# Kernel optimization log

Hardware: AMD Instinct MI355X
Metric: run time of the kernel (lower is better)

## Reference

```python
import jax, jax.numpy as jnp
import numpy as np

B, N, S, D, H = 64, 4096, 8, 256, 512
ITERS = 3
EPS = 1e-8      # slot-attention renormalize epsilon
LN_EPS = 1e-5   # torch LayerNorm default


def _ln(x, g, b):
    m = jnp.mean(x, -1, keepdims=True)
    v = jnp.mean((x - m) ** 2, -1, keepdims=True)
    return (x - m) * jax.lax.rsqrt(v + LN_EPS) * g + b


def setup_inputs() -> dict:
    key = jax.random.key(0)
    ks = jax.random.split(key, 12)

    def xav(k, shape):
        s = (6.0 / (shape[-2] + shape[-1])) ** 0.5
        return jax.random.uniform(k, shape, jnp.float32, -s, s)

    gru_s = 1.0 / (D ** 0.5)
    return {
        "inputs": jax.random.normal(ks[0], (B, N, D), jnp.float32),
        "init_noise": jax.random.normal(ks[1], (B, S, D), jnp.float32),
        "slots_mu": xav(ks[2], (1, 1, D)),
        "slots_log_sigma": xav(ks[3], (1, 1, D)),
        "ln_in_g": jnp.ones(D), "ln_in_b": jnp.zeros(D),
        "ln_slots_g": jnp.ones(D), "ln_slots_b": jnp.zeros(D),
        "ln_mlp_g": jnp.ones(D), "ln_mlp_b": jnp.zeros(D),
        "Wq": xav(ks[4], (D, D)),
        "Wk": xav(ks[5], (D, D)),
        "Wv": xav(ks[6], (D, D)),
        "W_ih": jax.random.uniform(ks[7], (3 * D, D), jnp.float32, -gru_s, gru_s),
        "W_hh": jax.random.uniform(ks[8], (3 * D, D), jnp.float32, -gru_s, gru_s),
        "b_ih": jnp.zeros(3 * D), "b_hh": jnp.zeros(3 * D),
        "W1": xav(ks[9], (H, D)), "b1": jnp.zeros(H),
        "W2": xav(ks[10], (D, H)), "b2": jnp.zeros(D),
    }


def reference(inputs, init_noise, slots_mu, slots_log_sigma,
              ln_in_g, ln_in_b, ln_slots_g, ln_slots_b, ln_mlp_g, ln_mlp_b,
              Wq, Wk, Wv, W_ih, W_hh, b_ih, b_hh, W1, b1, W2, b2):
    x = _ln(inputs, ln_in_g, ln_in_b)               # (B,N,D)
    k = jnp.einsum('bnd,ed->bne', x, Wk)             # (B,N,D)
    v = jnp.einsum('bnd,ed->bne', x, Wv)             # (B,N,D)
    slots = slots_mu + jnp.exp(slots_log_sigma) * init_noise  # (B,S,D)
    scale = D ** (-0.5)
    for _ in range(ITERS):
        prev = slots
        s = _ln(slots, ln_slots_g, ln_slots_b)
        q = jnp.einsum('bsd,ed->bse', s, Wq) * scale
        logits = jnp.einsum('bse,bne->bsn', q, k)    # (B,S,N)
        attn = jax.nn.softmax(logits, -1) + EPS
        attn = attn / jnp.sum(attn, -1, keepdims=True)
        upd = jnp.einsum('bsn,bne->bse', attn, v)    # (B,S,D)
        # GRUCell (torch semantics)
        gx = jnp.einsum('bsd,ed->bse', upd, W_ih) + b_ih
        gh = jnp.einsum('bsd,ed->bse', prev, W_hh) + b_hh
        xr, xz, xn = jnp.split(gx, 3, -1)
        hr, hz, hn = jnp.split(gh, 3, -1)
        r = jax.nn.sigmoid(xr + hr)
        z = jax.nn.sigmoid(xz + hz)
        n = jnp.tanh(xn + r * hn)
        slots = (1.0 - z) * n + z * prev
        # residual MLP
        m = _ln(slots, ln_mlp_g, ln_mlp_b)
        h1 = jax.nn.relu(jnp.einsum('bsd,hd->bsh', m, W1) + b1)
        slots = slots + jnp.einsum('bsh,dh->bsd', h1, W2) + b2
    return slots
```

## Files before the change

### kernel.cpp

```cpp
#include <hip/hip_runtime.h>

#define BB 64
#define NN 4096
#define SS 8
#define DD 256
#define HH 512
#define NCH 16
#define CHK 256
#define LSP2 260

typedef __attribute__((ext_vector_type(4))) float f32x4;
typedef __attribute__((ext_vector_type(8))) short short8;
typedef __attribute__((ext_vector_type(8))) __bf16 bf16x8;

static __device__ __forceinline__ f32x4 MFMA(short8 a, short8 b, f32x4 c){
  return __builtin_amdgcn_mfma_f32_16x16x32_bf16(
      __builtin_bit_cast(bf16x8, a), __builtin_bit_cast(bf16x8, b), c, 0, 0, 0);
}

static __device__ __forceinline__ unsigned short f2bf(float f){
  unsigned int x = __builtin_bit_cast(unsigned int, f);
  x += 0x7FFFu + ((x >> 16) & 1u);
  return (unsigned short)(x >> 16);
}

static __device__ __forceinline__ unsigned int pk2(float a, float b){
  return (unsigned int)f2bf(a) | ((unsigned int)f2bf(b) << 16);
}

__global__ __launch_bounds__(256, 4) void pre_kernel(
    const float* __restrict__ Wq, const float* __restrict__ Wk,
    const float* __restrict__ Wih, const float* __restrict__ Wv,
    float* __restrict__ wqkT, float* __restrict__ mf32)
{
  __shared__ float sh[256];
  const int blk = blockIdx.x, t = threadIdx.x;
  if(blk < 256){
    const int d2 = blk;
    sh[t] = Wk[(size_t)t * 256 + d2];
    __syncthreads();
    float acc = 0.f;
    #pragma unroll 8
    for(int e = 0; e < 256; ++e) acc += sh[e] * Wq[(size_t)e * 256 + t];
    wqkT[(size_t)d2 * 256 + t] = acc * 0.0625f;
  } else {
    const int e = blk - 256;
    sh[t] = Wih[(size_t)e * 256 + t];
    __syncthreads();
    float acc = 0.f;
    #pragma unroll 8
    for(int d = 0; d < 256; ++d) acc += sh[d] * Wv[(size_t)d * 256 + t];
    mf32[(size_t)e * 256 + t] = acc;
  }
}

struct PackDesc {
  const float* src[5];
  unsigned short* dst[5];
  int ET[5];
  int K[5];
  int blkStart[6];
};

__global__ void pack_all_kernel(PackDesc pd){
  int blk = blockIdx.x;
  int seg = 0;
  #pragma unroll
  for(int i = 1; i < 5; ++i) if(blk >= pd.blkStart[i]) seg = i;
  int tid = (blk - pd.blkStart[seg]) * 256 + threadIdx.x;
  int ET = pd.ET[seg], K = pd.K[seg];
  if(tid >= ET * 16 * K) return;
  int i    = tid & 7;
  int lane = (tid >> 3) & 63;
  int rest = tid >> 9;
  int et = rest % ET;
  int kk = rest / ET;
  int row = et * 16 + (lane & 15);
  int col = kk * 32 + ((lane >> 4) << 3) + i;
  pd.dst[seg][tid] = f2bf(pd.src[seg][(size_t)row * K + col]);
}

__global__ __launch_bounds__(256, 4) void ln_kernel(
    const float* __restrict__ inp, const float* __restrict__ g, const float* __restrict__ bta,
    unsigned short* __restrict__ x)
{
  const int t = threadIdx.x, w = t >> 6, l = t & 63;
  const size_t row0 = (size_t)blockIdx.x * 64;
  const int li = l & 15, lg = l >> 4;

  float4 gg[4], bb[4];
  #pragma unroll
  for(int q = 0; q < 4; ++q){
    gg[q] = ((const float4*)g)[li + q * 16];
    bb[q] = ((const float4*)bta)[li + q * 16];
  }
  #pragma unroll
  for(int rr = 0; rr < 4; ++rr){
    int r = w * 16 + rr * 4 + lg;
    const float4* rp = (const float4*)(inp + (row0 + r) * DD);
    float4 xv[4];
    #pragma unroll
    for(int q = 0; q < 4; ++q) xv[q] = rp[li + q * 16];
    float s1 = 0.f, s2 = 0.f;
    #pragma unroll
    for(int q = 0; q < 4; ++q){
      s1 += xv[q].x + xv[q].y + xv[q].z + xv[q].w;
      s2 += xv[q].x*xv[q].x + xv[q].y*xv[q].y + xv[q].z*xv[q].z + xv[q].w*xv[q].w;
    }
    #pragma unroll
    for(int o = 8; o >= 1; o >>= 1){ s1 += __shfl_xor(s1, o); s2 += __shfl_xor(s2, o); }
    float mean = s1 * (1.0f/256.0f);
    float inv  = rsqrtf(s2 * (1.0f/256.0f) - mean*mean + 1e-5f);
    #pragma unroll
    for(int q = 0; q < 4; ++q){
      float y0 = (xv[q].x-mean)*inv*gg[q].x + bb[q].x;
      float y1 = (xv[q].y-mean)*inv*gg[q].y + bb[q].y;
      float y2 = (xv[q].z-mean)*inv*gg[q].z + bb[q].z;
      float y3 = (xv[q].w-mean)*inv*gg[q].w + bb[q].w;
      *(uint2*)((char*)x + (row0 + r) * 512 + q * 128 + li * 8) =
          make_uint2(pk2(y0,y1), pk2(y2,y3));
    }
  }
}

__global__ __launch_bounds__(256, 1) void init_kernel(
    const float* __restrict__ noise, const float* __restrict__ mu, const float* __restrict__ lsg,
    const float* __restrict__ lng, const float* __restrict__ lnb,
    const short8* __restrict__ wqkp, float* __restrict__ slots, float* __restrict__ qbuf)
{
  const int b = blockIdx.x, t = threadIdx.x, w = t >> 6, l = t & 63;
  __shared__ float SLN[SS * DD];
  __shared__ unsigned short A1[16 * DD];
  float muv = mu[t];
  float sgv = __expf(lsg[t]);
  #pragma unroll
  for(int s = 0; s < SS; ++s){
    float v = muv + sgv * noise[(size_t)b * 2048 + s * 256 + t];
    slots[(size_t)b * 2048 + s * 256 + t] = v;
    SLN[s * 256 + t] = v;
  }
  __syncthreads();
  float4 g4 = ((const float4*)lng)[l], bb4 = ((const float4*)lnb)[l];
  for(int sh = 0; sh < 2; ++sh){
    int s = w * 2 + sh;
    float4 x4 = ((const float4*)(SLN + s * 256))[l];
    float s1 = x4.x + x4.y + x4.z + x4.w;
    float s2 = x4.x*x4.x + x4.y*x4.y + x4.z*x4.z + x4.w*x4.w;
    #pragma unroll
    for(int o = 32; o >= 1; o >>= 1){ s1 += __shfl_xor(s1, o); s2 += __shfl_xor(s2, o); }
    float mean = s1 * (1.0f/256.0f);
    float inv  = rsqrtf(s2 * (1.0f/256.0f) - mean*mean + 1e-5f);
    float y0 = (x4.x-mean)*inv*g4.x + bb4.x;
    float y1 = (x4.y-mean)*inv*g4.y + bb4.y;
    float y2 = (x4.z-mean)*inv*g4.z + bb4.z;
    float y3 = (x4.w-mean)*inv*g4.w + bb4.w;
    int byte = s * 512 + ((l * 8) ^ ((s & 7) << 4));
    *(uint2*)((char*)A1 + byte) = make_uint2(pk2(y0,y1), pk2(y2,y3));
  }
  __syncthreads();
  const int m = l & 15;
  short8 af[8];
  #pragma unroll
  for(int kk = 0; kk < 8; ++kk){
    int ab = m * 512 + (((kk * 64) + ((l >> 4) << 4)) ^ ((m & 7) << 4));
    af[kk] = *(const short8*)((const char*)A1 + ab);
  }
  #pragma unroll
  for(int i = 0; i < 4; ++i){
    int et = w + i * 4;
    f32x4 c = (f32x4){0,0,0,0};
    #pragma unroll
    for(int kk = 0; kk < 8; ++kk) c = MFMA(af[kk], wqkp[((kk * 16 + et) << 6) + l], c);
    int e = et * 16 + (l & 15);
    #pragma unroll
    for(int j = 0; j < 4; ++j){
      int s = ((l >> 4) << 2) + j;
      if(s < 8) qbuf[(size_t)b * 2048 + s * 256 + e] = c[j];
    }
  }
}

__global__ __launch_bounds__(256, 3) void attn_kernel(
    const unsigned short* __restrict__ x_, const float* __restrict__ qbuf,
    float* __restrict__ pupd, float* __restrict__ pms)
{
  const int blk = blockIdx.x;
  const int b = blk >> 4, c = blk & 15;
  const int t = threadIdx.x, w = t >> 6, l = t & 63;
  __shared__ __align__(16) char SMEM[32768];
  float* ls = (float*)SMEM;
  char*  xv = SMEM;

  const int m = l & 15, lg = l >> 4;
  short8 aq[8];
  #pragma unroll
  for(int kk = 0; kk < 8; ++kk){
    if(m < 8){
      const float* qp = qbuf + (size_t)b * 2048 + m * 256 + kk * 32 + (lg << 3);
      float4 qa = *(const float4*)qp;
      float4 qb = *(const float4*)(qp + 4);
      int4 pv = make_int4((int)pk2(qa.x,qa.y), (int)pk2(qa.z,qa.w),
                          (int)pk2(qb.x,qb.y), (int)pk2(qb.z,qb.w));
      aq[kk] = __builtin_bit_cast(short8, pv);
    } else {
      aq[kk] = (short8){0,0,0,0,0,0,0,0};
    }
  }

  const unsigned short* xb = x_ + ((size_t)b * NN + (size_t)c * CHK) * DD;
  #pragma unroll
  for(int nt = 0; nt < 4; ++nt){
    int nb = w * 64 + nt * 16;
    f32x4 acc = (f32x4){0,0,0,0};
    #pragma unroll
    for(int kk = 0; kk < 8; ++kk){
      short8 bk = *(const short8*)(xb + (size_t)(nb + m) * DD + kk * 32 + (lg << 3));
      acc = MFMA(aq[kk], bk, acc);
    }
    if(l < 32){
      int s4 = lg * 4;
      #pragma unroll
      for(int j = 0; j < 4; ++j) ls[(s4 + j) * LSP2 + nb + m] = acc[j];
    }
  }
  __syncthreads();

  for(int sh = 0; sh < 2; ++sh){
    int s = w * 2 + sh;
    float* base = ls + s * LSP2;
    float4 v0 = *(float4*)(base + l * 4);
    float mx = fmaxf(fmaxf(v0.x,v0.y),fmaxf(v0.z,v0.w));
    #pragma unroll
    for(int o = 32; o >= 1; o >>= 1) mx = fmaxf(mx, __shfl_xor(mx, o));
    float e0 = __expf(v0.x-mx), e1 = __expf(v0.y-mx), e2 = __expf(v0.z-mx), e3 = __expf(v0.w-mx);
    float sm = e0+e1+e2+e3;
    #pragma unroll
    for(int o = 32; o >= 1; o >>= 1) sm += __shfl_xor(sm, o);
    *(float4*)(base + l * 4) = make_float4(e0,e1,e2,e3);
    if(l == 0){
      pms[(((size_t)b * 16 + c) * 8 + s) * 2    ] = mx;
      pms[(((size_t)b * 16 + c) * 8 + s) * 2 + 1] = sm;
    }
  }
  __syncthreads();

  short8 pa[8];
  #pragma unroll
  for(int kk = 0; kk < 8; ++kk){
    if(m < 8){
      const float* pp = ls + m * LSP2 + kk * 32 + (lg << 3);
      int4 pv = make_int4((int)pk2(pp[0],pp[1]), (int)pk2(pp[2],pp[3]),
                          (int)pk2(pp[4],pp[5]), (int)pk2(pp[6],pp[7]));
      pa[kk] = __builtin_bit_cast(short8, pv);
    } else {
      pa[kk] = (short8){0,0,0,0,0,0,0,0};
    }
  }
  __syncthreads();

  f32x4 acc[4];
  #pragma unroll
  for(int dt = 0; dt < 4; ++dt) acc[dt] = (f32x4){0,0,0,0};
  const int p = t & 31, db = t >> 5;

  uint4 va0, va1, va2, va3, vb0, vb1, vb2, vb3;
  {
    const unsigned short* rA = xb + (size_t)(2 * p) * DD + db * 32;
    const unsigned short* rB = rA + DD;
    va0 = *(const uint4*)(rA);      vb0 = *(const uint4*)(rB);
    va1 = *(const uint4*)(rA + 8);  vb1 = *(const uint4*)(rB + 8);
    va2 = *(const uint4*)(rA + 16); vb2 = *(const uint4*)(rB + 16);
    va3 = *(const uint4*)(rA + 24); vb3 = *(const uint4*)(rB + 24);
  }

  for(int ng = 0; ng < 4; ++ng){
    {
      uint4 VA[4] = {va0, va1, va2, va3};
      uint4 VB[4] = {vb0, vb1, vb2, vb3};
      #pragma unroll
      for(int q = 0; q < 4; ++q){
        unsigned int wa[4] = {VA[q].x, VA[q].y, VA[q].z, VA[q].w};
        unsigned int wb[4] = {VB[q].x, VB[q].y, VB[q].z, VB[q].w};
        #pragma unroll
        for(int h = 0; h < 4; ++h){
          int d0 = db * 32 + q * 8 + h * 2;
          unsigned int a = wa[h], bv = wb[h];
          unsigned int v0 = (a & 0xFFFFu) | (bv << 16);
          unsigned int v1 = (a >> 16) | (bv & 0xFFFF0000u);
          *(unsigned int*)(xv + d0 * 128 + ((p * 4) ^ ((d0 & 7) << 4))) = v0;
          int d1 = d0 + 1;
          *(unsigned int*)(xv + d1 * 128 + ((p * 4) ^ ((d1 & 7) << 4))) = v1;
        }
      }
    }
    if(ng < 3){
      const unsigned short* rA = xb + (size_t)((ng + 1) * 64 + 2 * p) * DD + db * 32;
      const unsigned short* rB = rA + DD;
      va0 = *(const uint4*)(rA);      vb0 = *(const uint4*)(rB);
      va1 = *(const uint4*)(rA + 8);  vb1 = *(const uint4*)(rB + 8);
      va2 = *(const uint4*)(rA + 16); vb2 = *(const uint4*)(rB + 16);
      va3 = *(const uint4*)(rA + 24); vb3 = *(const uint4*)(rB + 24);
    }
    __builtin_amdgcn_s_setprio(1);
    #pragma unroll
    for(int kkloc = 0; kkloc < 2; ++kkloc){
      int kk = ng * 2 + kkloc;
      #pragma unroll
      for(int dt = 0; dt < 4; ++dt){
        int d = w * 64 + dt * 16 + m;
        short8 bv = *(const short8*)(xv + d * 128 + ((kkloc * 64 + lg * 16) ^ ((d & 7) << 4)));
        acc[dt] = MFMA(pa[kk], bv, acc[dt]);
      }
    }
    __builtin_amdgcn_s_setprio(0);
  }
  if(l < 32){
    int s4 = lg * 4;
    #pragma unroll
    for(int dt = 0; dt < 4; ++dt){
      int d0 = w * 64 + dt * 16;
      #pragma unroll
      for(int j = 0; j < 4; ++j)
        pupd[((size_t)b * 16 + c) * 2048 + (s4 + j) * 256 + d0 + m] = acc[dt][j];
    }
  }
}

__global__ __launch_bounds__(1024, 1) void update_kernel(
    const float* __restrict__ pupd, const float* __restrict__ pms,
    float* __restrict__ slots, float* __restrict__ qbuf,
    const short8* __restrict__ mp, const short8* __restrict__ whh,
    const float* __restrict__ bih, const float* __restrict__ bhh,
    const short8* __restrict__ w1p, const float* __restrict__ b1v,
    const short8* __restrict__ w2p, const float* __restrict__ b2v,
    const float* __restrict__ lnsg, const float* __restrict__ lnsb,
    const float* __restrict__ lnmg, const float* __restrict__ lnmb,
    const short8* __restrict__ wqkp,
    float* __restrict__ dout, const int last)
{
  const int b = blockIdx.x, t = threadIdx.x, w = t >> 6, l = t & 63;
  __shared__ unsigned short A1[16 * 256];
  __shared__ unsigned short A2[16 * 256];
  __shared__ unsigned short A3[16 * 512];
  __shared__ float GR[8 * 256], GZ[8 * 256], GXN[8 * 256], GHN[8 * 256];
  __shared__ float SL[8 * 256];
  __shared__ float PMS[256];

  if(t < 256) PMS[t] = pms[(size_t)b * 256 + t];
  __syncthreads();

  const int col = t & 255, sg = t >> 8;
  float upd[2], pv[2];
  #pragma unroll
  for(int ss = 0; ss < 2; ++ss){
    int s = sg * 2 + ss;
    float mx = -1e30f;
    #pragma unroll
    for(int cc = 0; cc < 16; ++cc) mx = fmaxf(mx, PMS[(cc * 8 + s) * 2]);
    float Z = 0.f, u = 0.f;
    #pragma unroll
    for(int cc = 0; cc < 16; ++cc){
      float e = __expf(PMS[(cc * 8 + s) * 2] - mx);
      Z += e * PMS[(cc * 8 + s) * 2 + 1];
      u += e * pupd[((size_t)b * 16 + cc) * 2048 + s * 256 + col];
    }
    upd[ss] = u / Z;
    pv[ss]  = slots[(size_t)b * 2048 + s * 256 + col];
  }
  #pragma unroll
  for(int ss = 0; ss < 2; ++ss){
    int s = sg * 2 + ss;
    int byte = s * 512 + ((col * 2) ^ ((s & 7) << 4));
    *(unsigned short*)((char*)A1 + byte) = f2bf(upd[ss]);
    *(unsigned short*)((char*)A2 + byte) = f2bf(pv[ss]);
  }
  __syncthreads();

  {
    const int mq = l & 15;
    short8 a1f[8], a2f[8];
    #pragma unroll
    for(int kk = 0; kk < 8; ++kk){
      int ab = mq * 512 + (((kk * 64) + ((l >> 4) << 4)) ^ ((mq & 7) << 4));
      a1f[kk] = *(const short8*)((const char*)A1 + ab);
      a2f[kk] = *(const short8*)((const char*)A2 + ab);
    }
    #pragma unroll
    for(int i = 0; i < 3; ++i){
      int et = w + i * 16;
      f32x4 c1 = (f32x4){0,0,0,0}, c2 = (f32x4){0,0,0,0};
      #pragma unroll
      for(int kk = 0; kk < 8; ++kk){
        c1 = MFMA(a1f[kk], mp[((kk * 48 + et) << 6) + l], c1);
        c2 = MFMA(a2f[kk], whh[((kk * 48 + et) << 6) + l], c2);
      }
      int e = et * 16 + (l & 15);
      float xb = bih[e], hb = bhh[e];
      #pragma unroll
      for(int j = 0; j < 4; ++j){
        int s = ((l >> 4) << 2) + j;
        if(s < 8){
          float xx = c1[j] + xb, h = c2[j] + hb;
          if(i == 0)      GR[s * 256 + e      ] = 1.f/(1.f + __expf(-(xx + h)));
          else if(i == 1) GZ[s * 256 + (e-256)] = 1.f/(1.f + __expf(-(xx + h)));
          else { GXN[s * 256 + (e-512)] = xx; GHN[s * 256 + (e-512)] = h; }
        }
      }
    }
  }
  __syncthreads();

  #pragma unroll
  for(int ss = 0; ss < 2; ++ss){
    int s = sg * 2 + ss, idx = s * 256 + col;
    float r = GR[idx], z = GZ[idx], xn = GXN[idx], hn = GHN[idx];
    float nn = tanhf(xn + r * hn);
    SL[idx] = (1.f - z) * nn + z * pv[ss];
  }
  __syncthreads();

  if(w < 8){
    float4 g4 = ((const float4*)lnmg)[l], bb4 = ((const float4*)lnmb)[l];
    int s = w;
    float4 x4 = ((const float4*)(SL + s * 256))[l];
    float s1 = x4.x + x4.y + x4.z + x4.w;
    float s2 = x4.x*x4.x + x4.y*x4.y + x4.z*x4.z + x4.w*x4.w;
    #pragma unroll
    for(int o = 32; o >= 1; o >>= 1){ s1 += __shfl_xor(s1, o); s2 += __shfl_xor(s2, o); }
    float mean = s1 * (1.0f/256.0f);
    float inv  = rsqrtf(s2 * (1.0f/256.0f) - mean*mean + 1e-5f);
    float y0 = (x4.x-mean)*inv*g4.x + bb4.x;
    float y1 = (x4.y-mean)*inv*g4.y + bb4.y;
    float y2 = (x4.z-mean)*inv*g4.z + bb4.z;
    float y3 = (x4.w-mean)*inv*g4.w + bb4.w;
    int byte = s * 512 + ((l * 8) ^ ((s & 7) << 4));
    *(uint2*)((char*)A1 + byte) = make_uint2(pk2(y0,y1), pk2(y2,y3));
  }
  __syncthreads();

  {
    const int mq = l & 15;
    short8 af[8];
    #pragma unroll
    for(int kk = 0; kk < 8; ++kk){
      int ab = mq * 512 + (((kk * 64) + ((l >> 4) << 4)) ^ ((mq & 7) << 4));
      af[kk] = *(const short8*)((const char*)A1 + ab);
    }
    #pragma unroll
    for(int i = 0; i < 2; ++i){
      int et = w + i * 16;
      f32x4 cc = (f32x4){0,0,0,0};
      #pragma unroll
      for(int kk = 0; kk < 8; ++kk) cc = MFMA(af[kk], w1p[((kk * 32 + et) << 6) + l], cc);
      int e = et * 16 + (l & 15);
      float bb = b1v[e];
      #pragma unroll
      for(int j = 0; j < 4; ++j){
        int s = ((l >> 4) << 2) + j;
        if(s < 8){
          float h = fmaxf(cc[j] + bb, 0.f);
          int byte = s * 1024 + ((e * 2) ^ ((s & 7) << 4));
          *(unsigned short*)((char*)A3 + byte) = f2bf(h);
        }
      }
    }
  }
  __syncthreads();

  {
    const int mq = l & 15;
    short8 af[16];
    #pragma unroll
    for(int kk = 0; kk < 16; ++kk){
      int ab = mq * 1024 + (((kk * 64) + ((l >> 4) << 4)) ^ ((mq & 7) << 4));
      af[kk] = *(const short8*)((const char*)A3 + ab);
    }
    {
      int et = w;
      f32x4 cc = (f32x4){0,0,0,0};
      #pragma unroll
      for(int kk = 0; kk < 16; ++kk) cc = MFMA(af[kk], w2p[((kk * 16 + et) << 6) + l], cc);
      int e = et * 16 + (l & 15);
      float bb = b2v[e];
      #pragma unroll
      for(int j = 0; j < 4; ++j){
        int s = ((l >> 4) << 2) + j;
        if(s < 8) GR[s * 256 + e] = SL[s * 256 + e] + cc[j] + bb;
      }
    }
  }
  __syncthreads();

  for(int i = t; i < 2048; i += 1024){
    float v = GR[i];
    slots[(size_t)b * 2048 + i] = v;
    if(last) dout[(size_t)b * 2048 + i] = v;
  }
  if(w < 8){
    float4 g4 = ((const float4*)lnsg)[l], bb4 = ((const float4*)lnsb)[l];
    int s = w;
    float4 x4 = ((const float4*)(GR + s * 256))[l];
    float s1 = x4.x + x4.y + x4.z + x4.w;
    float s2 = x4.x*x4.x + x4.y*x4.y + x4.z*x4.z + x4.w*x4.w;
    #pragma unroll
    for(int o = 32; o >= 1; o >>= 1){ s1 += __shfl_xor(s1, o); s2 += __shfl_xor(s2, o); }
    float mean = s1 * (1.0f/256.0f);
    float inv  = rsqrtf(s2 * (1.0f/256.0f) - mean*mean + 1e-5f);
    float y0 = (x4.x-mean)*inv*g4.x + bb4.x;
    float y1 = (x4.y-mean)*inv*g4.y + bb4.y;
    float y2 = (x4.z-mean)*inv*g4.z + bb4.z;
    float y3 = (x4.w-mean)*inv*g4.w + bb4.w;
    int byte = s * 512 + ((l * 8) ^ ((s & 7) << 4));
    *(uint2*)((char*)A1 + byte) = make_uint2(pk2(y0,y1), pk2(y2,y3));
  }
  __syncthreads();
  {
    const int mq = l & 15;
    short8 af[8];
    #pragma unroll
    for(int kk = 0; kk < 8; ++kk){
      int ab = mq * 512 + (((kk * 64) + ((l >> 4) << 4)) ^ ((mq & 7) << 4));
      af[kk] = *(const short8*)((const char*)A1 + ab);
    }
    {
      int et = w;
      f32x4 cc = (f32x4){0,0,0,0};
      #pragma unroll
      for(int kk = 0; kk < 8; ++kk) cc = MFMA(af[kk], wqkp[((kk * 16 + et) << 6) + l], cc);
      int e = et * 16 + (l & 15);
      #pragma unroll
      for(int j = 0; j < 4; ++j){
        int s = ((l >> 4) << 2) + j;
        if(s < 8) qbuf[(size_t)b * 2048 + s * 256 + e] = cc[j];
      }
    }
  }
}

extern "C" void kernel_launch(void* const* d_in, const int* in_sizes, int n_in,
                              void* d_out, int out_size, void* d_ws, size_t ws_size,
                              hipStream_t stream)
{
  const float* inp   = (const float*)d_in[0];
  const float* noise = (const float*)d_in[1];
  const float* mu    = (const float*)d_in[2];
  const float* lsg   = (const float*)d_in[3];
  const float* lngi  = (const float*)d_in[4];
  const float* lnbi  = (const float*)d_in[5];
  const float* lngs  = (const float*)d_in[6];
  const float* lnbs  = (const float*)d_in[7];
  const float* lngm  = (const float*)d_in[8];
  const float* lnbm  = (const float*)d_in[9];
  const float* Wq    = (const float*)d_in[10];
  const float* Wk    = (const float*)d_in[11];
  const float* Wv    = (const float*)d_in[12];
  const float* Wih   = (const float*)d_in[13];
  const float* Whh   = (const float*)d_in[14];
  const float* bih   = (const float*)d_in[15];
  const float* bhh   = (const float*)d_in[16];
  const float* W1    = (const float*)d_in[17];
  const float* b1    = (const float*)d_in[18];
  const float* W2    = (const float*)d_in[19];
  const float* b2    = (const float*)d_in[20];
  float* dout = (float*)d_out;

  char* ws = (char*)d_ws;
  size_t off = 0;
  unsigned short* x   = (unsigned short*)(ws + off); off += (size_t)BB*NN*DD*2;
  short8* wqkp= (short8*)(ws + off); off += (size_t)256*256*2;
  short8* mp  = (short8*)(ws + off); off += (size_t)768*256*2;
  short8* whhp= (short8*)(ws + off); off += (size_t)768*256*2;
  short8* w1p = (short8*)(ws + off); off += (size_t)512*256*2;
  short8* w2p = (short8*)(ws + off); off += (size_t)256*512*2;
  float* wqkT = (float*)(ws + off);  off += (size_t)256*256*4;
  float* mf32 = (float*)(ws + off);  off += (size_t)768*256*4;
  float* qbuf = (float*)(ws + off);  off += (size_t)512*256*4;
  float* slots= (float*)(ws + off);  off += (size_t)512*256*4;
  float* pupd = (float*)(ws + off);  off += (size_t)BB*NCH*2048*4;
  float* pms  = (float*)(ws + off);  off += (size_t)BB*NCH*8*2*4;

  pre_kernel<<<1024, 256, 0, stream>>>(Wq, Wk, Wih, Wv, wqkT, mf32);

  PackDesc pd;
  const float* srcs[5] = {wqkT, mf32, Whh, W1, W2};
  unsigned short* dsts[5] = {(unsigned short*)wqkp, (unsigned short*)mp,
                             (unsigned short*)whhp, (unsigned short*)w1p,
                             (unsigned short*)w2p};
  int ets[5] = {16, 48, 48, 32, 16};
  int ks [5] = {256, 256, 256, 256, 512};
  int cum = 0;
  for(int i = 0; i < 5; ++i){
    pd.src[i] = srcs[i]; pd.dst[i] = dsts[i]; pd.ET[i] = ets[i]; pd.K[i] = ks[i];
    pd.blkStart[i] = cum;
    cum += (ets[i] * 16 * ks[i] + 255) / 256;
  }
  pd.blkStart[5] = cum;
  pack_all_kernel<<<cum, 256, 0, stream>>>(pd);

  ln_kernel<<<4096, 256, 0, stream>>>(inp, lngi, lnbi, x);
  init_kernel<<<64, 256, 0, stream>>>(noise, mu, lsg, lngs, lnbs, wqkp, slots, qbuf);

  for(int it = 0; it < 3; ++it){
    attn_kernel<<<BB * NCH, 256, 0, stream>>>(x, qbuf, pupd, pms);
    update_kernel<<<64, 1024, 0, stream>>>(pupd, pms, slots, qbuf, mp, whhp,
        bih, bhh, w1p, b1, w2p, b2, lngs, lnbs, lngm, lnbm, wqkp, dout, (it == 2) ? 1 : 0);
  }
}
```

Measured before the change: 338.2 us.

## Split attention over 64 chunks of 64 tokens per batch

Changes the split-softmax attention from 16 chunks of 256 tokens to 64 chunks of 64 tokens, so the attention grid grows from 1024 to 4096 blocks. Each block now does a single 16-row logits tile and a single staged V load, with no software-pipelined prefetch loop. The update kernel merges 64 partial max/sum/update sets instead of 16. This trades more launch parallelism and shorter per-block latency for four times the partial-update traffic written to and read back from global memory, plus a longer reduction in the update kernel.

```diff
diff --git a/kernel.cpp b/kernel.cpp
--- a/kernel.cpp
+++ b/kernel.cpp
@@ -5,9 +5,9 @@
 #define SS 8
 #define DD 256
 #define HH 512
-#define NCH 16
-#define CHK 256
-#define LSP2 260
+#define NCH 64
+#define CHK 64
+#define LSP3 68
 
 typedef __attribute__((ext_vector_type(4))) float f32x4;
 typedef __attribute__((ext_vector_type(8))) short short8;
@@ -185,7 +185,7 @@
     float* __restrict__ pupd, float* __restrict__ pms)
 {
   const int blk = blockIdx.x;
-  const int b = blk >> 4, c = blk & 15;
+  const int b = blk >> 6, c = blk & 63;
   const int t = threadIdx.x, w = t >> 6, l = t & 63;
   __shared__ __align__(16) char SMEM[32768];
   float* ls = (float*)SMEM;
@@ -208,9 +208,8 @@
   }
 
   const unsigned short* xb = x_ + ((size_t)b * NN + (size_t)c * CHK) * DD;
-  #pragma unroll
-  for(int nt = 0; nt < 4; ++nt){
-    int nb = w * 64 + nt * 16;
+  {
+    int nb = w * 16;
     f32x4 acc = (f32x4){0,0,0,0};
     #pragma unroll
     for(int kk = 0; kk < 8; ++kk){
@@ -220,35 +219,34 @@
     if(l < 32){
       int s4 = lg * 4;
       #pragma unroll
-      for(int j = 0; j < 4; ++j) ls[(s4 + j) * LSP2 + nb + m] = acc[j];
+      for(int j = 0; j < 4; ++j) ls[(s4 + j) * LSP3 + nb + m] = acc[j];
     }
   }
   __syncthreads();
 
   for(int sh = 0; sh < 2; ++sh){
     int s = w * 2 + sh;
-    float* base = ls + s * LSP2;
-    float4 v0 = *(float4*)(base + l * 4);
-    float mx = fmaxf(fmaxf(v0.x,v0.y),fmaxf(v0.z,v0.w));
+    float v = ls[s * LSP3 + l];
+    float mx = v;
     #pragma unroll
     for(int o = 32; o >= 1; o >>= 1) mx = fmaxf(mx, __shfl_xor(mx, o));
-    float e0 = __expf(v0.x-mx), e1 = __expf(v0.y-mx), e2 = __expf(v0.z-mx), e3 = __expf(v0.w-mx);
-    float sm = e0+e1+e2+e3;
+    float e0 = __expf(v - mx);
+    float sm = e0;
     #pragma unroll
     for(int o = 32; o >= 1; o >>= 1) sm += __shfl_xor(sm, o);
-    *(float4*)(base + l * 4) = make_float4(e0,e1,e2,e3);
+    ls[s * LSP3 + l] = e0;
     if(l == 0){
-      pms[(((size_t)b * 16 + c) * 8 + s) * 2    ] = mx;
-      pms[(((size_t)b * 16 + c) * 8 + s) * 2 + 1] = sm;
-    }
-  }
-  __syncthreads();
-
-  short8 pa[8];
-  #pragma unroll
-  for(int kk = 0; kk < 8; ++kk){
+      pms[(((size_t)b * 64 + c) * 8 + s) * 2    ] = mx;
+      pms[(((size_t)b * 64 + c) * 8 + s) * 2 + 1] = sm;
+    }
+  }
+  __syncthreads();
+
+  short8 pa[2];
+  #pragma unroll
+  for(int kk = 0; kk < 2; ++kk){
     if(m < 8){
-      const float* pp = ls + m * LSP2 + kk * 32 + (lg << 3);
+      const float* pp = ls + m * LSP3 + kk * 32 + (lg << 3);
       int4 pv = make_int4((int)pk2(pp[0],pp[1]), (int)pk2(pp[2],pp[3]),
                           (int)pk2(pp[4],pp[5]), (int)pk2(pp[6],pp[7]));
       pa[kk] = __builtin_bit_cast(short8, pv);
@@ -262,58 +260,42 @@
   #pragma unroll
   for(int dt = 0; dt < 4; ++dt) acc[dt] = (f32x4){0,0,0,0};
   const int p = t & 31, db = t >> 5;
-
-  uint4 va0, va1, va2, va3, vb0, vb1, vb2, vb3;
   {
     const unsigned short* rA = xb + (size_t)(2 * p) * DD + db * 32;
     const unsigned short* rB = rA + DD;
-    va0 = *(const uint4*)(rA);      vb0 = *(const uint4*)(rB);
-    va1 = *(const uint4*)(rA + 8);  vb1 = *(const uint4*)(rB + 8);
-    va2 = *(const uint4*)(rA + 16); vb2 = *(const uint4*)(rB + 16);
-    va3 = *(const uint4*)(rA + 24); vb3 = *(const uint4*)(rB + 24);
-  }
-
-  for(int ng = 0; ng < 4; ++ng){
-    {
-      uint4 VA[4] = {va0, va1, va2, va3};
-      uint4 VB[4] = {vb0, vb1, vb2, vb3};
-      #pragma unroll
-      for(int q = 0; q < 4; ++q){
-        unsigned int wa[4] = {VA[q].x, VA[q].y, VA[q].z, VA[q].w};
-        unsigned int wb[4] = {VB[q].x, VB[q].y, VB[q].z, VB[q].w};
-        #pragma unroll
-        for(int h = 0; h < 4; ++h){
-          int d0 = db * 32 + q * 8 + h * 2;
-          unsigned int a = wa[h], bv = wb[h];
-          unsigned int v0 = (a & 0xFFFFu) | (bv << 16);
-          unsigned int v1 = (a >> 16) | (bv & 0xFFFF0000u);
-          *(unsigned int*)(xv + d0 * 128 + ((p * 4) ^ ((d0 & 7) << 4))) = v0;
-          int d1 = d0 + 1;
-          *(unsigned int*)(xv + d1 * 128 + ((p * 4) ^ ((d1 & 7) << 4))) = v1;
-        }
+    uint4 VA[4], VB[4];
+    VA[0] = *(const uint4*)(rA);      VB[0] = *(const uint4*)(rB);
+    VA[1] = *(const uint4*)(rA + 8);  VB[1] = *(const uint4*)(rB + 8);
+    VA[2] = *(const uint4*)(rA + 16); VB[2] = *(const uint4*)(rB + 16);
+    VA[3] = *(const uint4*)(rA + 24); VB[3] = *(const uint4*)(rB + 24);
+    #pragma unroll
+    for(int q = 0; q < 4; ++q){
+      unsigned int wa[4] = {VA[q].x, VA[q].y, VA[q].z, VA[q].w};
+      unsigned int wb[4] = {VB[q].x, VB[q].y, VB[q].z, VB[q].w};
+      #pragma unroll
+      for(int h = 0; h < 4; ++h){
+        int d0 = db * 32 + q * 8 + h * 2;
+        unsigned int a = wa[h], bv = wb[h];
+        unsigned int v0 = (a & 0xFFFFu) | (bv << 16);
+        unsigned int v1 = (a >> 16) | (bv & 0xFFFF0000u);
+        *(unsigned int*)(xv + d0 * 128 + ((p * 4) ^ ((d0 & 7) << 4))) = v0;
+        int d1 = d0 + 1;
+        *(unsigned int*)(xv + d1 * 128 + ((p * 4) ^ ((d1 & 7) << 4))) = v1;
       }
     }
-    if(ng < 3){
-      const unsigned short* rA = xb + (size_t)((ng + 1) * 64 + 2 * p) * DD + db * 32;
-      const unsigned short* rB = rA + DD;
-      va0 = *(const uint4*)(rA);      vb0 = *(const uint4*)(rB);
-      va1 = *(const uint4*)(rA + 8);  vb1 = *(const uint4*)(rB + 8);
-      va2 = *(const uint4*)(rA + 16); vb2 = *(const uint4*)(rB + 16);
-      va3 = *(const uint4*)(rA + 24); vb3 = *(const uint4*)(rB + 24);
-    }
-    __builtin_amdgcn_s_setprio(1);
-    #pragma unroll
-    for(int kkloc = 0; kkloc < 2; ++kkloc){
-      int kk = ng * 2 + kkloc;
-      #pragma unroll
-      for(int dt = 0; dt < 4; ++dt){
-        int d = w * 64 + dt * 16 + m;
-        short8 bv = *(const short8*)(xv + d * 128 + ((kkloc * 64 + lg * 16) ^ ((d & 7) << 4)));
-        acc[dt] = MFMA(pa[kk], bv, acc[dt]);
-      }
-    }
-    __builtin_amdgcn_s_setprio(0);
-  }
+  }
+  __builtin_amdgcn_s_setprio(1);
+  #pragma unroll
+  for(int kkloc = 0; kkloc < 2; ++kkloc){
+    #pragma unroll
+    for(int dt = 0; dt < 4; ++dt){
+      int d = w * 64 + dt * 16 + m;
+      short8 bv = *(const short8*)(xv + d * 128 + ((kkloc * 64 + lg * 16) ^ ((d & 7) << 4)));
+      acc[dt] = MFMA(pa[kkloc], bv, acc[dt]);
+    }
+  }
+  __builtin_amdgcn_s_setprio(0);
+
   if(l < 32){
     int s4 = lg * 4;
     #pragma unroll
@@ -321,7 +303,7 @@
       int d0 = w * 64 + dt * 16;
       #pragma unroll
       for(int j = 0; j < 4; ++j)
-        pupd[((size_t)b * 16 + c) * 2048 + (s4 + j) * 256 + d0 + m] = acc[dt][j];
+        pupd[((size_t)b * 64 + c) * 2048 + (s4 + j) * 256 + d0 + m] = acc[dt][j];
     }
   }
 }
@@ -344,9 +326,9 @@
   __shared__ unsigned short A3[16 * 512];
   __shared__ float GR[8 * 256], GZ[8 * 256], GXN[8 * 256], GHN[8 * 256];
   __shared__ float SL[8 * 256];
-  __shared__ float PMS[256];
-
-  if(t < 256) PMS[t] = pms[(size_t)b * 256 + t];
+  __shared__ float PMS[1024];
+
+  PMS[t] = pms[(size_t)b * 1024 + t];
   __syncthreads();
 
   const int col = t & 255, sg = t >> 8;
@@ -355,14 +337,14 @@
   for(int ss = 0; ss < 2; ++ss){
     int s = sg * 2 + ss;
     float mx = -1e30f;
-    #pragma unroll
-    for(int cc = 0; cc < 16; ++cc) mx = fmaxf(mx, PMS[(cc * 8 + s) * 2]);
+    #pragma unroll 8
+    for(int cc = 0; cc < 64; ++cc) mx = fmaxf(mx, PMS[(cc * 8 + s) * 2]);
     float Z = 0.f, u = 0.f;
-    #pragma unroll
-    for(int cc = 0; cc < 16; ++cc){
+    #pragma unroll 8
+    for(int cc = 0; cc < 64; ++cc){
       float e = __expf(PMS[(cc * 8 + s) * 2] - mx);
       Z += e * PMS[(cc * 8 + s) * 2 + 1];
-      u += e * pupd[((size_t)b * 16 + cc) * 2048 + s * 256 + col];
+      u += e * pupd[((size_t)b * 64 + cc) * 2048 + s * 256 + col];
     }
     upd[ss] = u / Z;
     pv[ss]  = slots[(size_t)b * 2048 + s * 256 + col];
```

After: 420.2 us. +24.3%, slower.
